# Performance work log

Hardware: AMD Instinct MI355X
Metric: run time of the kernel (lower is better)

Reference implementation:

```python
import jax, jax.numpy as jnp
import numpy as np

#   per angular channel l: out_l = (1/sqrt(2l+1)) * sum_m x_nu[n,m,q] * x_1[n,m,p]
#   stacked over l with zero padding in the m axis (pad beyond 2l+1 is zero,
#   so the m-sum is unaffected), features flattened as full (q, p) outer product.

L = 4       # l = 0..3
N = 50000   # atomic environments (samples)
M = 7       # 2*l_max + 1
F_NU = 32   # features of density_nu per l
F_1 = 16    # features of density_1 per l


def setup_inputs() -> dict:
    key = jax.random.key(0)
    k1, k2 = jax.random.split(key)
    x_nu = jax.random.normal(k1, (L, N, M, F_NU), dtype=jnp.float32)
    x_1 = jax.random.normal(k2, (L, N, M, F_1), dtype=jnp.float32)
    ls = jnp.arange(L)
    # mask m-components beyond 2l+1 for each l  -> [L, M]
    mmask = (jnp.arange(M)[None, :] < (2 * ls + 1)[:, None]).astype(jnp.float32)
    x_nu = x_nu * mmask[:, None, :, None]
    x_1 = x_1 * mmask[:, None, :, None]
    return {"x_nu": x_nu, "x_1": x_1}


def reference(x_nu, x_1):
    # x_nu: [L, N, M, F_nu], x_1: [L, N, M, F_1]
    l_dim, n, _, f_nu = x_nu.shape
    f_1 = x_1.shape[-1]
    cg = 1.0 / jnp.sqrt(2.0 * jnp.arange(l_dim, dtype=jnp.float32) + 1.0)  # [L]
    # full (q_nu, q_1) outer product with sum over m, per l
    out = jnp.einsum('lnmq,lnmp->nlqp', x_nu, x_1)  # [N, L, F_nu, F_1]
    out = out * cg[None, :, None, None]
    return out.reshape(n, l_dim * f_nu * f_1)  # [N, L*F_nu*F_1]
```

## Files before the change

### kernel.cpp

```cpp
#include <hip/hip_runtime.h>


constexpr int L_DIM  = 4;
constexpr int M_DIM  = 7;
constexpr int FNU    = 32;
constexpr int F1     = 16;
constexpr int XNU_W  = L_DIM * M_DIM * FNU;
constexpr int X1_W   = L_DIM * M_DIM * F1;
constexpr int SAMP_W = XNU_W + X1_W;
constexpr int OUT_W  = L_DIM * FNU * F1;

__global__ __launch_bounds__(256) void ps_kernel(
    const float* __restrict__ x_nu,
    const float* __restrict__ x_1,
    float* __restrict__ out,
    int N)
{
    __shared__ float lds[2 * SAMP_W];
    const int t  = threadIdx.x;
    const int n0 = blockIdx.x * 2;

    const float4* __restrict__ xnu4 = reinterpret_cast<const float4*>(x_nu);
    const float4* __restrict__ x14  = reinterpret_cast<const float4*>(x_1);
    float4* lds4 = reinterpret_cast<float4*>(lds);

    #pragma unroll
    for (int ii = 0; ii < 3; ++ii) {
        int i = t + ii * 256;
        if (i < 2 * 336) {
            int s = (i >= 336) ? 1 : 0;
            int r = i - s * 336;
            int n = n0 + s;
            if (n < N) {
                float4 v; int dst;
                if (r < 224) {
                    int l = r / 56, off = r - l * 56;
                    v   = xnu4[(size_t)(l * N + n) * 56 + off];
                    dst = s * (SAMP_W / 4) + l * 56 + off;
                } else {
                    int r2 = r - 224;
                    int l = r2 / 28, off = r2 - l * 28;
                    v   = x14[(size_t)(l * N + n) * 28 + off];
                    dst = s * (SAMP_W / 4) + (XNU_W / 4) + l * 28 + off;
                }
                lds4[dst] = v;
            }
        }
    }
    __syncthreads();

    const int s  = t >> 7;
    const int u7 = t & 127;
    const int l  = u7 >> 5;
    const int u  = u7 & 31;
    const int pb = (u & 3) * 4;
    const int q2 = u >> 2;

    const int n = n0 + s;
    if (n >= N) return;

    const float* xnu_s = lds + s * SAMP_W + l * (M_DIM * FNU);
    const float* x1_s  = lds + s * SAMP_W + XNU_W + l * (M_DIM * F1);

    float acc[4][4];
    #pragma unroll
    for (int k = 0; k < 4; ++k)
        #pragma unroll
        for (int j = 0; j < 4; ++j) acc[k][j] = 0.0f;

    #pragma unroll
    for (int m = 0; m < M_DIM; ++m) {
        float4 b = *reinterpret_cast<const float4*>(&x1_s[m * F1 + pb]);
        float a[4];
        #pragma unroll
        for (int k = 0; k < 4; ++k) a[k] = xnu_s[m * FNU + q2 + 8 * k];
        #pragma unroll
        for (int k = 0; k < 4; ++k) {
            acc[k][0] += a[k] * b.x;
            acc[k][1] += a[k] * b.y;
            acc[k][2] += a[k] * b.z;
            acc[k][3] += a[k] * b.w;
        }
    }

    const float scale = rsqrtf(2.0f * (float)l + 1.0f);
    float* outp = out + (size_t)n * OUT_W + l * (FNU * F1);
    #pragma unroll
    for (int k = 0; k < 4; ++k) {
        int q = q2 + 8 * k;
        float4 v = make_float4(acc[k][0] * scale, acc[k][1] * scale,
                               acc[k][2] * scale, acc[k][3] * scale);
        *reinterpret_cast<float4*>(&outp[q * F1 + pb]) = v;
    }
}

extern "C" void kernel_launch(void* const* d_in, const int* in_sizes, int n_in,
                              void* d_out, int out_size, void* d_ws, size_t ws_size,
                              hipStream_t stream) {
    const float* x_nu = (const float*)d_in[0];
    const float* x_1  = (const float*)d_in[1];
    float* out = (float*)d_out;
    const int N = in_sizes[0] / XNU_W;
    const int blocks = (N + 1) / 2;
    ps_kernel<<<blocks, 256, 0, stream>>>(x_nu, x_1, out, N);
}
```

Before: 565.5 us.

## Load inputs directly to LDS, process four samples per block, nontemporal stores

Each block now handles four samples instead of two, and each thread loops over two samples in the compute phase. Input staging uses global_load_lds to write straight into shared memory without going through registers, and out-of-range samples are clamped rather than skipped. Output writes become nontemporal stores so the large streaming output does not pollute cache. The aim is lower load latency and register use for this memory-bound kernel. The cost is more LDS per block, which can lower occupancy.

```diff
diff --git a/kernel.cpp b/kernel.cpp
--- a/kernel.cpp
+++ b/kernel.cpp
@@ -9,6 +9,11 @@
 constexpr int X1_W   = L_DIM * M_DIM * F1;
 constexpr int SAMP_W = XNU_W + X1_W;
 constexpr int OUT_W  = L_DIM * FNU * F1;
+constexpr int SPB    = 4;
+constexpr int NV4    = SPB * SAMP_W / 4;
+constexpr int NCHUNK = NV4 / 64;
+
+typedef float f32x4 __attribute__((ext_vector_type(4)));
 
 __global__ __launch_bounds__(256) void ps_kernel(
     const float* __restrict__ x_nu,
@@ -16,81 +21,87 @@
     float* __restrict__ out,
     int N)
 {
-    __shared__ float lds[2 * SAMP_W];
-    const int t  = threadIdx.x;
-    const int n0 = blockIdx.x * 2;
+    __shared__ float lds[SPB * SAMP_W];
+    const int t    = threadIdx.x;
+    const int n0   = blockIdx.x * SPB;
+    const int lane = t & 63;
+    const int wid  = t >> 6;
 
     const float4* __restrict__ xnu4 = reinterpret_cast<const float4*>(x_nu);
     const float4* __restrict__ x14  = reinterpret_cast<const float4*>(x_1);
     float4* lds4 = reinterpret_cast<float4*>(lds);
 
     #pragma unroll
-    for (int ii = 0; ii < 3; ++ii) {
-        int i = t + ii * 256;
-        if (i < 2 * 336) {
-            int s = (i >= 336) ? 1 : 0;
+    for (int j = 0; j < 6; ++j) {
+        const int c = wid + 4 * j;
+        if (c < NCHUNK) {
+            const int i = c * 64 + lane;
+            int s = i / 336;
             int r = i - s * 336;
             int n = n0 + s;
-            if (n < N) {
-                float4 v; int dst;
-                if (r < 224) {
-                    int l = r / 56, off = r - l * 56;
-                    v   = xnu4[(size_t)(l * N + n) * 56 + off];
-                    dst = s * (SAMP_W / 4) + l * 56 + off;
-                } else {
-                    int r2 = r - 224;
-                    int l = r2 / 28, off = r2 - l * 28;
-                    v   = x14[(size_t)(l * N + n) * 28 + off];
-                    dst = s * (SAMP_W / 4) + (XNU_W / 4) + l * 28 + off;
-                }
-                lds4[dst] = v;
+            if (n >= N) n = N - 1;
+            const float4* src;
+            if (r < 224) {
+                int l = r / 56, off = r - l * 56;
+                src = &xnu4[(size_t)(l * N + n) * 56 + off];
+            } else {
+                int r2 = r - 224;
+                int l = r2 / 28, off = r2 - l * 28;
+                src = &x14[(size_t)(l * N + n) * 28 + off];
             }
+            __builtin_amdgcn_global_load_lds(
+                (const __attribute__((address_space(1))) void*)src,
+                (__attribute__((address_space(3))) void*)&lds4[i],
+                16, 0, 0);
         }
     }
     __syncthreads();
 
-    const int s  = t >> 7;
     const int u7 = t & 127;
     const int l  = u7 >> 5;
     const int u  = u7 & 31;
     const int pb = (u & 3) * 4;
     const int q2 = u >> 2;
-
-    const int n = n0 + s;
-    if (n >= N) return;
-
-    const float* xnu_s = lds + s * SAMP_W + l * (M_DIM * FNU);
-    const float* x1_s  = lds + s * SAMP_W + XNU_W + l * (M_DIM * F1);
-
-    float acc[4][4];
-    #pragma unroll
-    for (int k = 0; k < 4; ++k)
-        #pragma unroll
-        for (int j = 0; j < 4; ++j) acc[k][j] = 0.0f;
+    const float scale = rsqrtf(2.0f * (float)l + 1.0f);
 
     #pragma unroll
-    for (int m = 0; m < M_DIM; ++m) {
-        float4 b = *reinterpret_cast<const float4*>(&x1_s[m * F1 + pb]);
-        float a[4];
-        #pragma unroll
-        for (int k = 0; k < 4; ++k) a[k] = xnu_s[m * FNU + q2 + 8 * k];
-        #pragma unroll
-        for (int k = 0; k < 4; ++k) {
-            acc[k][0] += a[k] * b.x;
-            acc[k][1] += a[k] * b.y;
-            acc[k][2] += a[k] * b.z;
-            acc[k][3] += a[k] * b.w;
+    for (int ss = 0; ss < 2; ++ss) {
+        const int s = (t >> 7) + 2 * ss;
+        const int n = n0 + s;
+        if (n < N) {
+            const float* xnu_s = lds + s * SAMP_W + l * (M_DIM * FNU);
+            const float* x1_s  = lds + s * SAMP_W + XNU_W + l * (M_DIM * F1);
+
+            float acc[4][4];
+            #pragma unroll
+            for (int k = 0; k < 4; ++k)
+                #pragma unroll
+                for (int j = 0; j < 4; ++j) acc[k][j] = 0.0f;
+
+            #pragma unroll
+            for (int m = 0; m < M_DIM; ++m) {
+                float4 b = *reinterpret_cast<const float4*>(&x1_s[m * F1 + pb]);
+                float a[4];
+                #pragma unroll
+                for (int k = 0; k < 4; ++k) a[k] = xnu_s[m * FNU + q2 + 8 * k];
+                #pragma unroll
+                for (int k = 0; k < 4; ++k) {
+                    acc[k][0] += a[k] * b.x;
+                    acc[k][1] += a[k] * b.y;
+                    acc[k][2] += a[k] * b.z;
+                    acc[k][3] += a[k] * b.w;
+                }
+            }
+
+            float* outp = out + (size_t)n * OUT_W + l * (FNU * F1);
+            #pragma unroll
+            for (int k = 0; k < 4; ++k) {
+                int q = q2 + 8 * k;
+                f32x4 v = { acc[k][0] * scale, acc[k][1] * scale,
+                            acc[k][2] * scale, acc[k][3] * scale };
+                __builtin_nontemporal_store(v, reinterpret_cast<f32x4*>(&outp[q * F1 + pb]));
+            }
         }
-    }
-
-    const float scale = rsqrtf(2.0f * (float)l + 1.0f);
-    float* outp = out + (size_t)n * OUT_W + l * (FNU * F1);
-    #pragma unroll
-    for (int k = 0; k < 4; ++k) {
-        int q = q2 + 8 * k;
-        float4 v = make_float4(acc[k][0] * scale, acc[k][1] * scale,
-                               acc[k][2] * scale, acc[k][3] * scale);
-        *reinterpret_cast<float4*>(&outp[q * F1 + pb]) = v;
     }
 }
 
@@ -101,6 +112,6 @@
     const float* x_1  = (const float*)d_in[1];
     float* out = (float*)d_out;
     const int N = in_sizes[0] / XNU_W;
-    const int blocks = (N + 1) / 2;
+    const int blocks = (N + SPB - 1) / SPB;
     ps_kernel<<<blocks, 256, 0, stream>>>(x_nu, x_1, out, N);
 }
```

Result: slower. 580.8 us (+2.7%).
